# Kernel optimization log

Measured on AMD Instinct MI355X. Metric: run time of the kernel, lower is better.

The kernel has to match this reference:

```python
import jax, jax.numpy as jnp
import numpy as np

B, N, DIM = 4, 4096, 1024
HEADS, DIM_HEAD = 16, 64
DIM_INNER = HEADS * DIM_HEAD
ATTN_SCALE = 8.0
EPS = 1e-12  # F.normalize default eps


def setup_inputs() -> dict:
    key = jax.random.key(0)
    k1, k2, k3, k4, k5 = jax.random.split(key, 5)
    x = jax.random.normal(k1, (B, N, DIM), dtype=jnp.float32)
    gamma = jnp.ones((DIM,), dtype=jnp.float32)
    # stored as (in, out) so forward is x @ w
    w_qkv = jax.random.normal(k2, (DIM, 3 * DIM_INNER), dtype=jnp.float32) * (DIM ** -0.5)
    temperature = jnp.ones((HEADS, 1, 1), dtype=jnp.float32)
    w_out = jax.random.normal(k3, (DIM_INNER, DIM), dtype=jnp.float32) * (DIM_INNER ** -0.5)
    return {"x": x, "gamma": gamma, "w_qkv": w_qkv, "temperature": temperature, "w_out": w_out}


def _l2norm(t):
    # F.normalize(t, dim=-1): t / max(||t||_2, eps)
    n = jnp.linalg.norm(t, axis=-1, keepdims=True)
    return t / jnp.maximum(n, EPS)


def reference(x, gamma, w_qkv, temperature, w_out):
    b, n, dim = x.shape
    # RMSNorm: F.normalize(x, dim=-1) * sqrt(dim) * gamma
    xn = _l2norm(x) * (dim ** 0.5) * gamma
    # QKV projection -> qkv b h d n
    qkv = (xn @ w_qkv).reshape(b, n, 3, HEADS, DIM_HEAD)
    qkv = qkv.transpose(2, 0, 3, 4, 1)  # (3, b, h, d, n)
    q, k, v = qkv[0], qkv[1], qkv[2]
    # l2-normalize q, k over the sequence (last) axis; temperature-scale q
    q = _l2norm(q) * jnp.exp(temperature)  # temperature: (h,1,1) broadcast
    k = _l2norm(k)
    # cross-covariance attention over the small channel dim d
    sim = jnp.einsum('bhdn,bhen->bhde', q, k) * ATTN_SCALE
    attn = jax.nn.softmax(sim, axis=-1)
    out = jnp.einsum('bhde,bhen->bhdn', attn, v)
    # b h d n -> b n (h d), then out projection
    out = out.transpose(0, 3, 1, 2).reshape(b, n, DIM_INNER)
    return out @ w_out
```

## Files before the change

kernel.cpp:

```cpp
#include <hip/hip_runtime.h>
#include <stdint.h>

typedef unsigned short u16;
typedef unsigned int u32;
typedef __attribute__((ext_vector_type(8))) __bf16 bf16x8;
typedef __attribute__((ext_vector_type(4))) float f32x4;

#define M_TOT 16384
#define DIMX  1024

__device__ __forceinline__ u16 f2b(float f) {
  u32 u = __builtin_bit_cast(u32, f);
  u32 r = (u + 0x7fffu + ((u >> 16) & 1u)) >> 16;
  return (u16)r;
}

__device__ __forceinline__ void gl2lds16(const void* g, void* l) {
  __builtin_amdgcn_global_load_lds((const __attribute__((address_space(1))) void*)g,
                                   (__attribute__((address_space(3))) void*)l,
                                   16, 0, 0);
}

__global__ __launch_bounds__(256) void k_rms(const float* __restrict__ x,
                                             const float* __restrict__ gamma,
                                             u16* __restrict__ xn) {
  int row = blockIdx.x;
  int t = threadIdx.x;
  const float4* xr = (const float4*)(x + (size_t)row * DIMX);
  float4 v = xr[t];
  float ss = v.x * v.x + v.y * v.y + v.z * v.z + v.w * v.w;
#pragma unroll
  for (int o = 32; o > 0; o >>= 1) ss += __shfl_xor(ss, o, 64);
  __shared__ float wss[4];
  int w = t >> 6;
  if ((t & 63) == 0) wss[w] = ss;
  __syncthreads();
  float tot = wss[0] + wss[1] + wss[2] + wss[3];
  float scale = 32.0f / fmaxf(sqrtf(tot), 1e-12f);
  float4 g = ((const float4*)gamma)[t];
  ushort4 o4;
  o4.x = f2b(v.x * scale * g.x);
  o4.y = f2b(v.y * scale * g.y);
  o4.z = f2b(v.z * scale * g.z);
  o4.w = f2b(v.w * scale * g.w);
  ((ushort4*)xn)[(size_t)row * 256 + t] = o4;
}

__global__ __launch_bounds__(256) void k_castT(const float* __restrict__ in,
                                               u16* __restrict__ out, int Rr, int Cc) {
  __shared__ float tile[32][33];
  int c0 = blockIdx.x * 32, r0 = blockIdx.y * 32;
  int tx = threadIdx.x, ty = threadIdx.y;
#pragma unroll
  for (int i = 0; i < 4; i++)
    tile[ty + i * 8][tx] = in[(size_t)(r0 + ty + i * 8) * Cc + c0 + tx];
  __syncthreads();
#pragma unroll
  for (int i = 0; i < 4; i++)
    out[(size_t)(c0 + ty + i * 8) * Rr + r0 + tx] = f2b(tile[tx][ty + i * 8]);
}


template<bool SWAP>
__device__ __forceinline__ f32x4 mf(bf16x8 a, bf16x8 b, f32x4 c) {
  return SWAP ? __builtin_amdgcn_mfma_f32_16x16x32_bf16(b, a, c, 0, 0, 0)
              : __builtin_amdgcn_mfma_f32_16x16x32_bf16(a, b, c, 0, 0, 0);
}

__device__ __forceinline__ void stage_half(const u16* __restrict__ g,
                                           u16* dst, int t, int k0) {
#pragma unroll
  for (int r = 0; r < 2; r++) {
    int chunk = r * 512 + t;
    int row = chunk >> 3;
    int cc = (chunk & 7) ^ (row & 7);
    gl2lds16(g + (size_t)row * 1024 + (k0 + cc * 8),
             dst + (r * 512 + (t >> 6) * 64) * 8);
  }
}

template<bool SWAP>
__device__ __forceinline__ void gemm_core256(const u16* __restrict__ Ag,
                                             const u16* __restrict__ Bg,
                                             u16* lds, int t, f32x4 (&acc)[8][4]) {
  const int lane = t & 63;
  const int r16 = lane & 15, q = lane >> 4;
  const int wr = (t >> 6) >> 2, wc = (t >> 6) & 3;
  const int s0 = (q ^ (r16 & 7)) * 8;
  const int arow = wr * 16 + r16;
  const int brow = wc * 16 + r16;

  stage_half(Ag,              lds + 0 * 8192, t, 0);
  stage_half(Bg,              lds + 2 * 8192, t, 0);
  stage_half(Bg + 128 * 1024, lds + 3 * 8192, t, 0);
  stage_half(Ag + 128 * 1024, lds + 1 * 8192, t, 0);
  asm volatile("s_waitcnt vmcnt(4)" ::: "memory");
  __builtin_amdgcn_s_barrier();

  bf16x8 af[4][2], bl[2][2], bh[2][2];
#pragma unroll 1
  for (int tt = 0; tt < 16; tt++) {
    const int bo = (tt & 1) << 15;
    const int nb = bo ^ 32768;
    const int k1 = ((tt + 1) & 15) << 6;
    const u16* A0 = lds + bo;
    const u16* A1 = lds + bo + 8192;
    const u16* B0 = lds + bo + 16384;
    const u16* B1 = lds + bo + 24576;

#pragma unroll
    for (int i = 0; i < 4; i++) {
      af[i][0] = *(const bf16x8*)(A0 + (i * 32 + arow) * 64 + s0);
      af[i][1] = *(const bf16x8*)(A0 + (i * 32 + arow) * 64 + (s0 ^ 32));
    }
#pragma unroll
    for (int j = 0; j < 2; j++) {
      bl[j][0] = *(const bf16x8*)(B0 + (j * 64 + brow) * 64 + s0);
      bl[j][1] = *(const bf16x8*)(B0 + (j * 64 + brow) * 64 + (s0 ^ 32));
    }
    stage_half(Ag, lds + nb + 0 * 8192, t, k1);
    __builtin_amdgcn_s_setprio(1);
#pragma unroll
    for (int kq = 0; kq < 2; kq++)
#pragma unroll
      for (int i = 0; i < 4; i++)
#pragma unroll
        for (int j = 0; j < 2; j++)
          acc[i][j] = mf<SWAP>(af[i][kq], bl[j][kq], acc[i][j]);
    __builtin_amdgcn_s_setprio(0);
    asm volatile("s_waitcnt vmcnt(4)" ::: "memory");
    __builtin_amdgcn_s_barrier();

#pragma unroll
    for (int j = 0; j < 2; j++) {
      bh[j][0] = *(const bf16x8*)(B1 + (j * 64 + brow) * 64 + s0);
      bh[j][1] = *(const bf16x8*)(B1 + (j * 64 + brow) * 64 + (s0 ^ 32));
    }
    stage_half(Bg, lds + nb + 2 * 8192, t, k1);
    __builtin_amdgcn_s_setprio(1);
#pragma unroll
    for (int kq = 0; kq < 2; kq++)
#pragma unroll
      for (int i = 0; i < 4; i++)
#pragma unroll
        for (int j = 0; j < 2; j++)
          acc[i][2 + j] = mf<SWAP>(af[i][kq], bh[j][kq], acc[i][2 + j]);
    __builtin_amdgcn_s_setprio(0);
    asm volatile("s_waitcnt vmcnt(4)" ::: "memory");
    __builtin_amdgcn_s_barrier();

#pragma unroll
    for (int i = 0; i < 4; i++) {
      af[i][0] = *(const bf16x8*)(A1 + (i * 32 + arow) * 64 + s0);
      af[i][1] = *(const bf16x8*)(A1 + (i * 32 + arow) * 64 + (s0 ^ 32));
    }
    stage_half(Bg + 128 * 1024, lds + nb + 3 * 8192, t, k1);
    __builtin_amdgcn_s_setprio(1);
#pragma unroll
    for (int kq = 0; kq < 2; kq++)
#pragma unroll
      for (int i = 0; i < 4; i++)
#pragma unroll
        for (int j = 0; j < 2; j++)
          acc[4 + i][j] = mf<SWAP>(af[i][kq], bl[j][kq], acc[4 + i][j]);
    __builtin_amdgcn_s_setprio(0);
    __builtin_amdgcn_s_barrier();

    stage_half(Ag + 128 * 1024, lds + nb + 1 * 8192, t, k1);
    __builtin_amdgcn_s_setprio(1);
#pragma unroll
    for (int kq = 0; kq < 2; kq++)
#pragma unroll
      for (int i = 0; i < 4; i++)
#pragma unroll
        for (int j = 0; j < 2; j++)
          acc[4 + i][2 + j] = mf<SWAP>(af[i][kq], bh[j][kq], acc[4 + i][2 + j]);
    __builtin_amdgcn_s_setprio(0);
    asm volatile("s_waitcnt vmcnt(4)" ::: "memory");
    __builtin_amdgcn_s_barrier();
  }
}

__global__ __launch_bounds__(512, 2) void k_gemm1(const u16* __restrict__ A,
                                                  const u16* __restrict__ Bt,
                                                  u16* __restrict__ qkT,
                                                  u16* __restrict__ vmat,
                                                  float* __restrict__ sumsq) {
  __shared__ u16 lds[8 * 8192];
  int l = blockIdx.x;
  int xcd = l & 7, c = l >> 3;
  int mt = xcd * 8 + (c & 7);
  int nt = c >> 3;
  int m0 = mt * 256, n0 = nt * 256;
  int t = threadIdx.x, lane = t & 63;
  int r16 = lane & 15, q = lane >> 4;
  int wr = (t >> 6) >> 2, wc = (t >> 6) & 3;
  f32x4 acc[8][4] = {};
  if (n0 < 2048) {
    gemm_core256<false>(A + (size_t)m0 * 1024, Bt + (size_t)n0 * 1024, lds, t, acc);
    int b = m0 >> 12;
#pragma unroll
    for (int j = 0; j < 4; j++) {
      int cc = n0 + j * 64 + wc * 16 + r16;
      float colss = 0.f;
#pragma unroll
      for (int i = 0; i < 8; i++) {
        f32x4 a = acc[i][j];
        colss += a.x * a.x + a.y * a.y + a.z * a.z + a.w * a.w;
        int m = m0 + i * 32 + wr * 16 + q * 4;
        ushort4 o4;
        o4.x = f2b(a.x); o4.y = f2b(a.y); o4.z = f2b(a.z); o4.w = f2b(a.w);
        *(ushort4*)(qkT + (size_t)cc * M_TOT + m) = o4;
      }
      colss += __shfl_xor(colss, 16, 64);
      colss += __shfl_xor(colss, 32, 64);
      if (lane < 16) atomicAdd(&sumsq[b * 2048 + cc], colss);
    }
  } else {
    gemm_core256<true>(A + (size_t)m0 * 1024, Bt + (size_t)n0 * 1024, lds, t, acc);
    int vc0 = n0 - 2048;
#pragma unroll
    for (int i = 0; i < 8; i++) {
      int m = m0 + i * 32 + wr * 16 + r16;
#pragma unroll
      for (int j = 0; j < 4; j++) {
        int cc = vc0 + j * 64 + wc * 16 + q * 4;
        f32x4 a = acc[i][j];
        ushort4 o4;
        o4.x = f2b(a.x); o4.y = f2b(a.y); o4.z = f2b(a.z); o4.w = f2b(a.w);
        *(ushort4*)(vmat + (size_t)m * 1024 + cc) = o4;
      }
    }
  }
}

__global__ __launch_bounds__(256) void k_attn_s(const u16* __restrict__ qkT,
                                                float* __restrict__ Spart) {
  int g = blockIdx.x, split = blockIdx.y;
  int t = threadIdx.x, lane = t & 63, w = t >> 6;
  int bh = g * 4 + w;
  int b = bh >> 4, h = bh & 15;
  int r16 = lane & 15, q = lane >> 4;
  const u16* qbase = qkT + (size_t)(h * 64) * M_TOT + b * 4096;
  const u16* kbase = qkT + (size_t)(1024 + h * 64) * M_TOT + b * 4096;
  f32x4 acc[4][4] = {};
#pragma unroll
  for (int it = 0; it < 8; it++) {
    int kk = split * 256 + it * 32 + q * 8;
    bf16x8 af[4], bfr[4];
#pragma unroll
    for (int i = 0; i < 4; i++) af[i] = *(const bf16x8*)(qbase + (size_t)(i * 16 + r16) * M_TOT + kk);
#pragma unroll
    for (int j = 0; j < 4; j++) bfr[j] = *(const bf16x8*)(kbase + (size_t)(j * 16 + r16) * M_TOT + kk);
#pragma unroll
    for (int i = 0; i < 4; i++)
#pragma unroll
      for (int j = 0; j < 4; j++)
        acc[i][j] = __builtin_amdgcn_mfma_f32_16x16x32_bf16(bfr[j], af[i], acc[i][j], 0, 0, 0);
  }
  float* Sp = Spart + ((size_t)split * 64 + bh) * 4096;
#pragma unroll
  for (int i = 0; i < 4; i++) {
    int d = i * 16 + r16;
#pragma unroll
    for (int j = 0; j < 4; j++) {
      int e = j * 16 + q * 4;
      *(f32x4*)(Sp + d * 64 + e) = acc[i][j];
    }
  }
}

__global__ __launch_bounds__(64) void k_softmax(const float* __restrict__ Spart,
                                                const float* __restrict__ sumsq,
                                                const float* __restrict__ temp,
                                                u16* __restrict__ PT) {
  int bh = blockIdx.x;
  int b = bh >> 4, h = bh & 15;
  int d = threadIdx.x;
  __shared__ float rnk[64];
  rnk[d] = 1.0f / fmaxf(sqrtf(sumsq[b * 2048 + 1024 + h * 64 + d]), 1e-12f);
  __syncthreads();
  float nq = sqrtf(sumsq[b * 2048 + h * 64 + d]);
  float qs = 8.0f * __expf(temp[h]) / fmaxf(nq, 1e-12f);
  const float* Sp = Spart + (size_t)bh * 4096 + d * 64;
  float vals[64];
#pragma unroll
  for (int e = 0; e < 64; e += 4) {
    f32x4 v = {};
#pragma unroll
    for (int s = 0; s < 16; s++)
      v += *(const f32x4*)(Sp + (size_t)s * 64 * 4096 + e);
    vals[e + 0] = v.x; vals[e + 1] = v.y; vals[e + 2] = v.z; vals[e + 3] = v.w;
  }
  float mx = -3.0e38f;
#pragma unroll
  for (int e = 0; e < 64; e++) {
    float v = vals[e] * qs * rnk[e];
    vals[e] = v;
    mx = fmaxf(mx, v);
  }
  float sum = 0.f;
#pragma unroll
  for (int e = 0; e < 64; e++) {
    float v = __expf(vals[e] - mx);
    vals[e] = v;
    sum += v;
  }
  float inv = 1.0f / sum;
#pragma unroll
  for (int e = 0; e < 64; e++)
    PT[((size_t)bh * 64 + e) * 64 + d] = f2b(vals[e] * inv);
}

__global__ __launch_bounds__(256) void k_m(const u16* __restrict__ woT,
                                           const u16* __restrict__ PT,
                                           u16* __restrict__ MT) {
  int bh = blockIdx.x;
  int b = bh >> 4, h = bh & 15;
  int o0 = blockIdx.y * 128;
  int t = threadIdx.x, lane = t & 63, w = t >> 6;
  int r16 = lane & 15, q = lane >> 4;
  const u16* pbase = PT + (size_t)bh * 4096;
  f32x4 acc[2][4] = {};
#pragma unroll
  for (int ks = 0; ks < 2; ks++) {
    int kk = ks * 32 + q * 8;
    bf16x8 af[2], bfr[4];
#pragma unroll
    for (int i = 0; i < 2; i++)
      af[i] = *(const bf16x8*)(woT + (size_t)(o0 + w * 32 + i * 16 + r16) * 1024 + h * 64 + kk);
#pragma unroll
    for (int j = 0; j < 4; j++)
      bfr[j] = *(const bf16x8*)(pbase + (size_t)(j * 16 + r16) * 64 + kk);
#pragma unroll
    for (int i = 0; i < 2; i++)
#pragma unroll
      for (int j = 0; j < 4; j++)
        acc[i][j] = __builtin_amdgcn_mfma_f32_16x16x32_bf16(af[i], bfr[j], acc[i][j], 0, 0, 0);
  }
  u16* dst = MT + (size_t)b * 1024 * 1024;
#pragma unroll
  for (int i = 0; i < 2; i++) {
    int o = o0 + w * 32 + i * 16 + q * 4;
#pragma unroll
    for (int j = 0; j < 4; j++) {
      int e = h * 64 + j * 16 + r16;
      f32x4 a = acc[i][j];
      dst[(size_t)(o + 0) * 1024 + e] = f2b(a.x);
      dst[(size_t)(o + 1) * 1024 + e] = f2b(a.y);
      dst[(size_t)(o + 2) * 1024 + e] = f2b(a.z);
      dst[(size_t)(o + 3) * 1024 + e] = f2b(a.w);
    }
  }
}

__global__ __launch_bounds__(512, 2) void k_gemm2(const u16* __restrict__ A,
                                                  const u16* __restrict__ Bt,
                                                  float* __restrict__ C) {
  __shared__ u16 lds[8 * 8192];
  int l = blockIdx.x;
  int xcd = l & 7, c = l >> 3;
  int mt = xcd * 8 + (c & 7);
  int nt = c >> 3;
  int m0 = mt * 256, n0 = nt * 256;
  int b = m0 >> 12;
  const u16* Bb = Bt + (size_t)b * 1024 * 1024;
  int t = threadIdx.x, lane = t & 63;
  int r16 = lane & 15, q = lane >> 4;
  int wr = (t >> 6) >> 2, wc = (t >> 6) & 3;
  f32x4 acc[8][4] = {};
  gemm_core256<true>(A + (size_t)m0 * 1024, Bb + (size_t)n0 * 1024, lds, t, acc);
#pragma unroll
  for (int i = 0; i < 8; i++) {
    int m = m0 + i * 32 + wr * 16 + r16;
#pragma unroll
    for (int j = 0; j < 4; j++) {
      int cc = n0 + j * 64 + wc * 16 + q * 4;
      *(f32x4*)(C + (size_t)m * 1024 + cc) = acc[i][j];
    }
  }
}

extern "C" void kernel_launch(void* const* d_in, const int* in_sizes, int n_in,
                              void* d_out, int out_size, void* d_ws, size_t ws_size,
                              hipStream_t stream) {
  const float* x     = (const float*)d_in[0];
  const float* gamma = (const float*)d_in[1];
  const float* wqkv  = (const float*)d_in[2];
  const float* temp  = (const float*)d_in[3];
  const float* wout  = (const float*)d_in[4];
  float* out = (float*)d_out;

  char* ws = (char*)d_ws;
  size_t off = 0;
  u16* xn = (u16*)(ws + off);    off += (size_t)M_TOT * 1024 * 2;
  u16* wqT = (u16*)(ws + off);   off += (size_t)3072 * 1024 * 2;
  u16* woT = (u16*)(ws + off);   off += (size_t)1024 * 1024 * 2;
  u16* qkT = (u16*)(ws + off);   off += (size_t)2048 * M_TOT * 2;
  u16* vmat = (u16*)(ws + off);  off += (size_t)M_TOT * 1024 * 2;
  float* sumsq = (float*)(ws + off); off += (size_t)4 * 2048 * 4;
  u16* PT = (u16*)(ws + off);    off += (size_t)64 * 64 * 64 * 2;
  u16* MT = (u16*)(ws + off);    off += (size_t)4 * 1024 * 1024 * 2;

  float* Spart = (float*)xn;

  hipMemsetAsync((void*)sumsq, 0, (size_t)4 * 2048 * 4, stream);

  k_rms<<<16384, 256, 0, stream>>>(x, gamma, xn);
  dim3 cb(32, 8);
  k_castT<<<dim3(3072 / 32, 1024 / 32), cb, 0, stream>>>(wqkv, wqT, 1024, 3072);
  k_castT<<<dim3(1024 / 32, 1024 / 32), cb, 0, stream>>>(wout, woT, 1024, 1024);
  k_gemm1<<<768, 512, 0, stream>>>(xn, wqT, qkT, vmat, sumsq);
  k_attn_s<<<dim3(16, 16), 256, 0, stream>>>(qkT, Spart);
  k_softmax<<<64, 64, 0, stream>>>(Spart, sumsq, temp, PT);
  k_m<<<dim3(64, 8), 256, 0, stream>>>(woT, PT, MT);
  k_gemm2<<<1024 / 4, 512, 0, stream>>>(vmat, MT, out);
}
```

Measured before the change: 324.7 us.

## Deepen GEMM LDS prefetch pipeline and parallelize softmax across four waves

The shared GEMM core now issues global-to-LDS loads for quarter-tiles up to two k-steps ahead, reusing the current buffer's freed quarters. This reorders barriers and waitcnts (vmcnt 6, plus lgkmcnt waits after barriers) to hide more global load latency behind MFMA work. Separately, the softmax kernel uses 256 threads per head, with each wave handling 16 columns, and reduces the max and sum through shared memory. The reordered buffer reuse carries a risk of races if the barrier placement is wrong, and the extra barriers add synchronization overhead.

New measurement: 329.0 us. No clear change (+1.3%).

```diff
diff --git a/kernel.cpp b/kernel.cpp
--- a/kernel.cpp
+++ b/kernel.cpp
@@ -85,16 +85,19 @@
                                              u16* lds, int t, f32x4 (&acc)[8][4]) {
   const int lane = t & 63;
   const int r16 = lane & 15, q = lane >> 4;
+  const int s0 = (q ^ (r16 & 7)) * 8;
   const int wr = (t >> 6) >> 2, wc = (t >> 6) & 3;
-  const int s0 = (q ^ (r16 & 7)) * 8;
   const int arow = wr * 16 + r16;
   const int brow = wc * 16 + r16;
 
-  stage_half(Ag,              lds + 0 * 8192, t, 0);
-  stage_half(Bg,              lds + 2 * 8192, t, 0);
-  stage_half(Bg + 128 * 1024, lds + 3 * 8192, t, 0);
-  stage_half(Ag + 128 * 1024, lds + 1 * 8192, t, 0);
-  asm volatile("s_waitcnt vmcnt(4)" ::: "memory");
+  stage_half(Ag,              lds + 0,     t, 0);
+  stage_half(Bg,              lds + 16384, t, 0);
+  stage_half(Bg + 128 * 1024, lds + 24576, t, 0);
+  stage_half(Ag + 128 * 1024, lds + 8192,  t, 0);
+  stage_half(Ag,              lds + 32768 + 0,     t, 64);
+  stage_half(Bg,              lds + 32768 + 16384, t, 64);
+  stage_half(Bg + 128 * 1024, lds + 32768 + 24576, t, 64);
+  asm volatile("s_waitcnt vmcnt(6)" ::: "memory");
   __builtin_amdgcn_s_barrier();
 
   bf16x8 af[4][2], bl[2][2], bh[2][2];
@@ -103,6 +106,7 @@
     const int bo = (tt & 1) << 15;
     const int nb = bo ^ 32768;
     const int k1 = ((tt + 1) & 15) << 6;
+    const int k2 = ((tt + 2) & 15) << 6;
     const u16* A0 = lds + bo;
     const u16* A1 = lds + bo + 8192;
     const u16* B0 = lds + bo + 16384;
@@ -118,7 +122,9 @@
       bl[j][0] = *(const bf16x8*)(B0 + (j * 64 + brow) * 64 + s0);
       bl[j][1] = *(const bf16x8*)(B0 + (j * 64 + brow) * 64 + (s0 ^ 32));
     }
-    stage_half(Ag, lds + nb + 0 * 8192, t, k1);
+    stage_half(Ag + 128 * 1024, lds + nb + 8192, t, k1);
+    __builtin_amdgcn_s_barrier();
+    asm volatile("s_waitcnt lgkmcnt(0)" ::: "memory");
     __builtin_amdgcn_s_setprio(1);
 #pragma unroll
     for (int kq = 0; kq < 2; kq++)
@@ -128,7 +134,6 @@
         for (int j = 0; j < 2; j++)
           acc[i][j] = mf<SWAP>(af[i][kq], bl[j][kq], acc[i][j]);
     __builtin_amdgcn_s_setprio(0);
-    asm volatile("s_waitcnt vmcnt(4)" ::: "memory");
     __builtin_amdgcn_s_barrier();
 
 #pragma unroll
@@ -136,7 +141,9 @@
       bh[j][0] = *(const bf16x8*)(B1 + (j * 64 + brow) * 64 + s0);
       bh[j][1] = *(const bf16x8*)(B1 + (j * 64 + brow) * 64 + (s0 ^ 32));
     }
-    stage_half(Bg, lds + nb + 2 * 8192, t, k1);
+    stage_half(Ag, lds + bo, t, k2);
+    __builtin_amdgcn_s_barrier();
+    asm volatile("s_waitcnt lgkmcnt(0)" ::: "memory");
     __builtin_amdgcn_s_setprio(1);
 #pragma unroll
     for (int kq = 0; kq < 2; kq++)
@@ -146,7 +153,6 @@
         for (int j = 0; j < 2; j++)
           acc[i][2 + j] = mf<SWAP>(af[i][kq], bh[j][kq], acc[i][2 + j]);
     __builtin_amdgcn_s_setprio(0);
-    asm volatile("s_waitcnt vmcnt(4)" ::: "memory");
     __builtin_amdgcn_s_barrier();
 
 #pragma unroll
@@ -154,7 +160,9 @@
       af[i][0] = *(const bf16x8*)(A1 + (i * 32 + arow) * 64 + s0);
       af[i][1] = *(const bf16x8*)(A1 + (i * 32 + arow) * 64 + (s0 ^ 32));
     }
-    stage_half(Bg + 128 * 1024, lds + nb + 3 * 8192, t, k1);
+    stage_half(Bg, lds + bo + 16384, t, k2);
+    __builtin_amdgcn_s_barrier();
+    asm volatile("s_waitcnt lgkmcnt(0)" ::: "memory");
     __builtin_amdgcn_s_setprio(1);
 #pragma unroll
     for (int kq = 0; kq < 2; kq++)
@@ -166,7 +174,7 @@
     __builtin_amdgcn_s_setprio(0);
     __builtin_amdgcn_s_barrier();
 
-    stage_half(Ag + 128 * 1024, lds + nb + 1 * 8192, t, k1);
+    stage_half(Bg + 128 * 1024, lds + bo + 24576, t, k2);
     __builtin_amdgcn_s_setprio(1);
 #pragma unroll
     for (int kq = 0; kq < 2; kq++)
@@ -176,7 +184,7 @@
         for (int j = 0; j < 2; j++)
           acc[4 + i][2 + j] = mf<SWAP>(af[i][kq], bh[j][kq], acc[4 + i][2 + j]);
     __builtin_amdgcn_s_setprio(0);
-    asm volatile("s_waitcnt vmcnt(4)" ::: "memory");
+    asm volatile("s_waitcnt vmcnt(6)" ::: "memory");
     __builtin_amdgcn_s_barrier();
   }
 }
@@ -270,22 +278,26 @@
   }
 }
 
-__global__ __launch_bounds__(64) void k_softmax(const float* __restrict__ Spart,
-                                                const float* __restrict__ sumsq,
-                                                const float* __restrict__ temp,
-                                                u16* __restrict__ PT) {
+__global__ __launch_bounds__(256) void k_softmax(const float* __restrict__ Spart,
+                                                 const float* __restrict__ sumsq,
+                                                 const float* __restrict__ temp,
+                                                 u16* __restrict__ PT) {
   int bh = blockIdx.x;
   int b = bh >> 4, h = bh & 15;
-  int d = threadIdx.x;
+  int t = threadIdx.x;
+  int d = t & 63, w = t >> 6;
+  int e0 = w * 16;
   __shared__ float rnk[64];
-  rnk[d] = 1.0f / fmaxf(sqrtf(sumsq[b * 2048 + 1024 + h * 64 + d]), 1e-12f);
+  __shared__ float redm[4][64];
+  __shared__ float reds[4][64];
+  if (t < 64) rnk[t] = 1.0f / fmaxf(sqrtf(sumsq[b * 2048 + 1024 + h * 64 + t]), 1e-12f);
   __syncthreads();
   float nq = sqrtf(sumsq[b * 2048 + h * 64 + d]);
   float qs = 8.0f * __expf(temp[h]) / fmaxf(nq, 1e-12f);
-  const float* Sp = Spart + (size_t)bh * 4096 + d * 64;
-  float vals[64];
-#pragma unroll
-  for (int e = 0; e < 64; e += 4) {
+  const float* Sp = Spart + (size_t)bh * 4096 + d * 64 + e0;
+  float vals[16];
+#pragma unroll
+  for (int e = 0; e < 16; e += 4) {
     f32x4 v = {};
 #pragma unroll
     for (int s = 0; s < 16; s++)
@@ -294,22 +306,27 @@
   }
   float mx = -3.0e38f;
 #pragma unroll
-  for (int e = 0; e < 64; e++) {
-    float v = vals[e] * qs * rnk[e];
+  for (int e = 0; e < 16; e++) {
+    float v = vals[e] * qs * rnk[e0 + e];
     vals[e] = v;
     mx = fmaxf(mx, v);
   }
-  float sum = 0.f;
-#pragma unroll
-  for (int e = 0; e < 64; e++) {
-    float v = __expf(vals[e] - mx);
+  redm[w][d] = mx;
+  __syncthreads();
+  float M = fmaxf(fmaxf(redm[0][d], redm[1][d]), fmaxf(redm[2][d], redm[3][d]));
+  float s = 0.f;
+#pragma unroll
+  for (int e = 0; e < 16; e++) {
+    float v = __expf(vals[e] - M);
     vals[e] = v;
-    sum += v;
-  }
-  float inv = 1.0f / sum;
-#pragma unroll
-  for (int e = 0; e < 64; e++)
-    PT[((size_t)bh * 64 + e) * 64 + d] = f2b(vals[e] * inv);
+    s += v;
+  }
+  reds[w][d] = s;
+  __syncthreads();
+  float inv = 1.0f / (reds[0][d] + reds[1][d] + reds[2][d] + reds[3][d]);
+#pragma unroll
+  for (int e = 0; e < 16; e++)
+    PT[((size_t)bh * 64 + e0 + e) * 64 + d] = f2b(vals[e] * inv);
 }
 
 __global__ __launch_bounds__(256) void k_m(const u16* __restrict__ woT,
@@ -412,7 +429,7 @@
   k_castT<<<dim3(1024 / 32, 1024 / 32), cb, 0, stream>>>(wout, woT, 1024, 1024);
   k_gemm1<<<768, 512, 0, stream>>>(xn, wqT, qkT, vmat, sumsq);
   k_attn_s<<<dim3(16, 16), 256, 0, stream>>>(qkT, Spart);
-  k_softmax<<<64, 64, 0, stream>>>(Spart, sumsq, temp, PT);
+  k_softmax<<<64, 256, 0, stream>>>(Spart, sumsq, temp, PT);
   k_m<<<dim3(64, 8), 256, 0, stream>>>(woT, PT, MT);
   k_gemm2<<<1024 / 4, 512, 0, stream>>>(vmat, MT, out);
 }
```
